# Kernel tuning notes

Measured on AMD Instinct MI355X. Metric: run time of the kernel, lower is better.

Reference implementation:

```python
import jax, jax.numpy as jnp
import numpy as np
from math import sqrt

HEAD_DIM = 128
MASKED = True


def setup_inputs() -> dict:
    key = jax.random.key(0)
    kq, kk, kv = jax.random.split(key, 3)
    B, S, D = 16, 2048, HEAD_DIM
    return {
        "queries": jax.random.normal(kq, (B, S, D), dtype=jnp.float32),
        "keys": jax.random.normal(kk, (B, S, D), dtype=jnp.float32),
        "values": jax.random.normal(kv, (B, S, D), dtype=jnp.float32),
    }


def reference(queries, keys, values):
    # scores: (B, Sq, Sk)
    scores = jnp.einsum("bqd,bkd->bqk", queries, keys) / sqrt(HEAD_DIM)
    if MASKED:
        # Faithful to torch.tril: upper-triangular entries set to 0.0
        # (NOT -inf) BEFORE softmax — reproduces the original's
        # multiplicative mask semantics exactly.
        scores = jnp.tril(scores)
    weights = jax.nn.softmax(scores, axis=-1)
    return jnp.einsum("bqk,bkd->bqd", weights, values)
```

## Files before the change

### kernel.cpp

```cpp
#include <hip/hip_runtime.h>
#include <hip/hip_bf16.h>

#define DEVI static __device__ __forceinline__

typedef __attribute__((ext_vector_type(8))) short short8;
typedef __attribute__((ext_vector_type(16))) float f32x16;
typedef __attribute__((ext_vector_type(2))) unsigned int uintx2;

#define S_LEN 2048
#define D_DIM 128
#define NBATCH 16
#define QSC ((float)(0.08838834764831845 * 1.4426950408889634))
#define MFIX 8.0f
#define E8 0.00390625f

#if __has_builtin(__builtin_amdgcn_exp2f)
#define EXP2(x) __builtin_amdgcn_exp2f(x)
#else
#define EXP2(x) exp2f(x)
#endif

DEVI unsigned short f2bf(float x) {
  union { float f; unsigned int u; } a; a.f = x;
  unsigned int u = a.u;
  unsigned int r = (u + 0x7fffu + ((u >> 16) & 1u)) >> 16;
  return (unsigned short)r;
}

DEVI unsigned int cvtpk(float lo, float hi) {
  unsigned int r;
  asm volatile("v_cvt_pk_bf16_f32 %0, %1, %2" : "=v"(r) : "v"(lo), "v"(hi));
  return r;
}

DEVI void plswap(unsigned int& a, unsigned int& b) {
  uintx2 r = __builtin_amdgcn_permlane32_swap(a, b, false, false);
  a = r[0];
  b = r[1];
}

DEVI float xhalf_sum(float x) {
  union { float f; unsigned int u; } a, b;
  a.f = x; b.f = x;
  plswap(a.u, b.u);
  return a.f + b.f;
}


__global__ void prep(const float* __restrict__ K, const float* __restrict__ V,
                     unsigned short* __restrict__ Kb, unsigned short* __restrict__ Vt,
                     float* __restrict__ Tsum) {
  __shared__ unsigned short t[64][68];
  const int tt = threadIdx.x;
  if (blockIdx.x >= 1024) {
    const int M4 = (NBATCH * S_LEN * D_DIM) / 4;
    for (int i = (blockIdx.x - 1024) * 256 + tt; i < M4; i += 2048 * 256) {
      const size_t idx = (size_t)i * 4;
      const float4 v = *reinterpret_cast<const float4*>(K + idx);
      ushort4 o;
      o.x = f2bf(v.x); o.y = f2bf(v.y); o.z = f2bf(v.z); o.w = f2bf(v.w);
      *reinterpret_cast<ushort4*>(Kb + idx) = o;
    }
    return;
  }
  const int bid = blockIdx.x;
  const int b = bid >> 6, rem = bid & 63;
  const int st = rem & 31, s0 = st * 64, d0 = (rem >> 5) * 64;
  const int r = tt >> 2, c = (tt & 3) * 16;
  const float* src = V + ((size_t)(b * S_LEN + s0 + r)) * D_DIM + d0 + c;
#pragma unroll
  for (int i = 0; i < 4; i++) {
    float4 v = reinterpret_cast<const float4*>(src)[i];
    t[r][c + 4 * i + 0] = f2bf(v.x);
    t[r][c + 4 * i + 1] = f2bf(v.y);
    t[r][c + 4 * i + 2] = f2bf(v.z);
    t[r][c + 4 * i + 3] = f2bf(v.w);
  }
  __syncthreads();
  unsigned short* dst = Vt + (((size_t)(b * 32 + st)) * 128 + d0 + r) * 64 + c;
#pragma unroll
  for (int i = 0; i < 4; i++) {
    ushort4 o;
    o.x = t[c + 4 * i + 0][r];
    o.y = t[c + 4 * i + 1][r];
    o.z = t[c + 4 * i + 2][r];
    o.w = t[c + 4 * i + 3][r];
    reinterpret_cast<ushort4*>(dst)[i] = o;
  }
  if (tt < 64) {
    float s = 0.0f;
#pragma unroll 8
    for (int rr = 0; rr < 64; rr++) {
      union { float f; unsigned int u; } cv;
      cv.u = ((unsigned int)t[rr][tt]) << 16;
      s += cv.f;
    }
    Tsum[((size_t)b * 32 + st) * 128 + d0 + tt] = s;
  }
}

__global__ void sufB(const float* __restrict__ Tsum, float* __restrict__ SufV) {
  const int b = blockIdx.x;
  const int d = threadIdx.x;
  float v[32];
#pragma unroll
  for (int t = 0; t < 32; t++) v[t] = Tsum[((size_t)b * 32 + t) * 128 + d];
  float run = 0.0f;
  SufV[((size_t)b * 33 + 32) * 128 + d] = 0.0f;
#pragma unroll
  for (int t = 31; t >= 0; t--) {
    run += v[t];
    SufV[((size_t)b * 33 + t) * 128 + d] = run;
  }
}


#define AS1 __attribute__((address_space(1)))
#define AS3 __attribute__((address_space(3)))

DEVI short8 ldK(const char* ldsK, int row, int off) {
  int addr = row * 256 + (off ^ ((row & 15) << 4));
  return *reinterpret_cast<const short8*>(ldsK + addr);
}
DEVI short8 ldV(const char* ldsV, int row, int off) {
  int addr = row * 128 + (off ^ ((row & 7) << 4));
  return *reinterpret_cast<const short8*>(ldsV + addr);
}

template <bool MASK>
DEVI void tile_body(const char* cb, const short8* qf, f32x16 (&acc)[4],
                    float& l_run, const int ln31, const int h, const int kh,
                    const int qrow, const int kvb) {
  f32x16 sT;
#pragma unroll
  for (int r = 0; r < 16; r++) sT[r] = 0.0f;
  __builtin_amdgcn_s_setprio(1);
#pragma unroll
  for (int kf = 0; kf < 8; kf++) {
    short8 af = ldK(cb, ln31 + 32 * kh, 32 * kf + 16 * h);
    sT = __builtin_amdgcn_mfma_f32_32x32x16_bf16(af, qf[kf], sT, 0, 0, 0);
  }
  __builtin_amdgcn_s_setprio(0);
  if (MASK) {
#pragma unroll
    for (int r = 0; r < 16; r++) {
      int kvg = kvb + (r & 3) + 8 * (r >> 2) + 4 * h;
      if (kvg > qrow) sT[r] = 0.0f;
    }
  }
#pragma unroll
  for (int r = 0; r < 16; r++) sT[r] = EXP2(sT[r] - MFIX);
  float ts[8];
#pragma unroll
  for (int r = 0; r < 8; r++) ts[r] = sT[r] + sT[r + 8];
#pragma unroll
  for (int r = 0; r < 4; r++) ts[r] = ts[r] + ts[r + 4];
  float sum = (ts[0] + ts[1]) + (ts[2] + ts[3]);
  sum = xhalf_sum(sum);
  l_run += sum;
#pragma unroll
  for (int kl = 0; kl < 2; kl++) {
    const int ra = 8 * kl;
    const int rb = 8 * kl + 4;
    unsigned int a0 = cvtpk(sT[ra + 0], sT[ra + 1]);
    unsigned int a1 = cvtpk(sT[ra + 2], sT[ra + 3]);
    unsigned int b0 = cvtpk(sT[rb + 0], sT[rb + 1]);
    unsigned int b1 = cvtpk(sT[rb + 2], sT[rb + 3]);
    plswap(a0, b0);
    plswap(a1, b1);
    union { short8 v; unsigned int u[4]; } pa;
    pa.u[0] = a0; pa.u[1] = a1; pa.u[2] = b0; pa.u[3] = b1;
    const int vboff = 64 * kh + 32 * kl + 16 * h;
    __builtin_amdgcn_s_setprio(1);
#pragma unroll
    for (int nt = 0; nt < 4; nt++) {
      short8 vb = ldV(cb + 16384, ln31 + 32 * nt, vboff);
      acc[nt] = __builtin_amdgcn_mfma_f32_32x32x16_bf16(pa.v, vb, acc[nt], 0, 0, 0);
    }
    __builtin_amdgcn_s_setprio(0);
  }
}

#define SMEM_BYTES 132096

struct WaveCtx {
  int w, lane, ln31, h, qs, grp, kh, tsel, dstpart;
  int off[8];
  const char* tbase;
};

DEVI void stage_tile(char* smem, const WaveCtx& c, int t, int j, int bi) {
  if (t <= j) {
    const char* src = c.tbase + (size_t)t * 16384;
    const int dbase = bi * 65536 + c.tsel * 32768 + c.dstpart;
#pragma unroll
    for (int i = 0; i < 8; i++) {
      __builtin_amdgcn_global_load_lds((const AS1 unsigned int*)(src + c.off[i]),
                                       (AS3 unsigned int*)(smem + dbase + i * 1024),
                                       16, 0, 0);
    }
  }
}

DEVI void run_strip(int j, int b, char* smem, const WaveCtx& c,
                    const float* __restrict__ Q, const float* __restrict__ SufV,
                    float* __restrict__ out) {
  const int q0 = j * 64;
  const int kv_end = q0 + 64;
  const int qrow = q0 + 32 * c.qs + c.ln31;

  short8 qf[8];
  {
    const float* qsrc = Q + ((size_t)b * S_LEN + qrow) * D_DIM + 8 * c.h;
#pragma unroll
    for (int kf = 0; kf < 8; kf++) {
      float4 a = *reinterpret_cast<const float4*>(qsrc + 16 * kf);
      float4 d = *reinterpret_cast<const float4*>(qsrc + 16 * kf + 4);
      union { short8 v; unsigned int u[4]; } q8;
      q8.u[0] = cvtpk(a.x * QSC, a.y * QSC);
      q8.u[1] = cvtpk(a.z * QSC, a.w * QSC);
      q8.u[2] = cvtpk(d.x * QSC, d.y * QSC);
      q8.u[3] = cvtpk(d.z * QSC, d.w * QSC);
      qf[kf] = q8.v;
    }
  }

  f32x16 acc[4];
#pragma unroll
  for (int nt = 0; nt < 4; nt++)
#pragma unroll
    for (int rr = 0; rr < 16; rr++) acc[nt][rr] = 0.0f;
  float l_run = 0.0f;

  const int nph = (j >> 1) + 1;
  stage_tile(smem, c, c.tsel, j, 0);
  __syncthreads();
  int bi = 0;
  for (int ph = 0; ph < nph; ph++) {
    if (ph + 1 < nph) stage_tile(smem, c, 2 * (ph + 1) + c.tsel, j, bi ^ 1);
    const int t = 2 * ph + c.grp;
    if (t <= j) {
      const char* cb = smem + bi * 65536 + c.grp * 32768;
      if (t == j)
        tile_body<true>(cb, qf, acc, l_run, c.ln31, c.h, c.kh, qrow,
                        t * 64 + 32 * c.kh);
      else
        tile_body<false>(cb, qf, acc, l_run, c.ln31, c.h, c.kh, qrow,
                         t * 64 + 32 * c.kh);
    }
    __syncthreads();
    bi ^= 1;
  }

  float* pbase = (float*)smem + c.w * 4096;
#pragma unroll
  for (int nt = 0; nt < 4; nt++)
#pragma unroll
    for (int rr = 0; rr < 16; rr++) {
      int cr = (rr & 3) + 8 * (rr >> 2) + 4 * c.h;
      pbase[cr * 128 + c.ln31 + 32 * nt] = acc[nt][rr];
    }
  float* lbase = (float*)(smem + 131072) + c.w * 32;
  if (c.h == 0) lbase[c.ln31] = l_run;
  __syncthreads();

  const int s = c.w & 3;
  const float* P0 = (float*)smem + (c.qs * 4) * 4096;
  const float* L0 = (float*)(smem + 131072) + (c.qs * 4) * 32;
  float l_tot = L0[c.ln31] + L0[32 + c.ln31] + L0[64 + c.ln31] + L0[96 + c.ln31];
  l_tot += (float)(S_LEN - kv_end) * E8;
  const float svv = SufV[((size_t)b * 33 + (kv_end >> 6)) * 128 + 32 * s + c.ln31];
  float* ob = out + ((size_t)b * S_LEN + q0 + 32 * c.qs) * D_DIM + 32 * s + c.ln31;
#pragma unroll
  for (int rr = 0; rr < 16; rr++) {
    int cr = (rr & 3) + 8 * (rr >> 2) + 4 * c.h;
    int cidx = cr * 128 + 32 * s + c.ln31;
    float v = P0[cidx] + P0[4096 + cidx] + P0[8192 + cidx] + P0[12288 + cidx];
    float lq = __shfl(l_tot, cr);
    ob[(size_t)cr * D_DIM] = (v + E8 * svv) / lq;
  }
  __syncthreads();
}

__global__ __launch_bounds__(512, 2) void attn_kernel(
    const float* __restrict__ Q, const unsigned short* __restrict__ Kb,
    const unsigned short* __restrict__ Vt, const float* __restrict__ SufV,
    float* __restrict__ out) {
  __shared__ __align__(16) char smem[SMEM_BYTES];

  WaveCtx c;
  const int tid = threadIdx.x;
  c.w = tid >> 6;
  c.lane = tid & 63;
  c.ln31 = c.lane & 31;
  c.h = c.lane >> 5;
  c.qs = c.w >> 2;
  c.grp = (c.w >> 1) & 1;
  c.kh = c.w & 1;
  c.tsel = c.w >> 2;
  const int part = c.w & 3;

  const int bid = blockIdx.x;
  const int x = bid & 7, idx = bid >> 3;
  const int b = 2 * x + (idx & 1);
  const int p = idx >> 1;

  if (part < 2) {
#pragma unroll
    for (int i = 0; i < 8; i++) {
      int L = (part * 8 + i) * 1024 + c.lane * 16;
      int row = L >> 8;
      c.off[i] = row * 256 + ((L & 255) ^ ((row & 15) << 4));
    }
    c.tbase = (const char*)(Kb + (size_t)b * S_LEN * D_DIM);
    c.dstpart = part * 8192;
  } else {
#pragma unroll
    for (int i = 0; i < 8; i++) {
      int L = ((part - 2) * 8 + i) * 1024 + c.lane * 16;
      int row = L >> 7;
      c.off[i] = (L & ~127) + ((L & 127) ^ ((row & 7) << 4));
    }
    c.tbase = (const char*)Vt + (size_t)b * (S_LEN * D_DIM * 2);
    c.dstpart = 16384 + (part - 2) * 8192;
  }

  run_strip(31 - p, b, smem, c, Q, SufV, out);
  run_strip(p, b, smem, c, Q, SufV, out);
}


extern "C" void kernel_launch(void* const* d_in, const int* in_sizes, int n_in,
                              void* d_out, int out_size, void* d_ws, size_t ws_size,
                              hipStream_t stream) {
  const float* Q = (const float*)d_in[0];
  const float* K = (const float*)d_in[1];
  const float* V = (const float*)d_in[2];
  float* out = (float*)d_out;

  char* ws = (char*)d_ws;
  unsigned short* Kb = (unsigned short*)ws;
  unsigned short* Vt = Kb + 4194304;
  float* Tsum = (float*)(ws + 16777216);
  float* SufV = Tsum + 65536;

  prep<<<3072, 256, 0, stream>>>(K, V, Kb, Vt, Tsum);
  sufB<<<16, 128, 0, stream>>>(Tsum, SufV);
  attn_kernel<<<256, 512, 0, stream>>>(Q, Kb, Vt, SufV, out);
}
```

Before: 53.12 us.

## Split paired causal strips into one-strip 256-thread blocks with single-tile pipeline

The old kernel ran 512-thread blocks that each processed two complementary query strips (31-p and p), with two wave groups working on alternate key tiles and a 4-way cross-wave reduction through LDS. The new kernel launches 512 blocks of 256 threads, one strip per block, streams one K/V tile at a time with double buffering, and reduces only two key-halves, adding one partial directly from registers. This halves LDS use and shrinks the epilogue reduction. The cost is that per-block work now varies a lot across causal strips, so load balance depends on the hardware scheduler, and each wave walks twice as many tiles serially.

```diff
diff --git a/kernel.cpp b/kernel.cpp
--- a/kernel.cpp
+++ b/kernel.cpp
@@ -181,37 +181,67 @@
   }
 }
 
-#define SMEM_BYTES 132096
-
-struct WaveCtx {
-  int w, lane, ln31, h, qs, grp, kh, tsel, dstpart;
+#define SMEM_BYTES 66048
+
+__global__ __launch_bounds__(256, 2) void attn_kernel(
+    const float* __restrict__ Q, const unsigned short* __restrict__ Kb,
+    const unsigned short* __restrict__ Vt, const float* __restrict__ SufV,
+    float* __restrict__ out) {
+  __shared__ __align__(16) char smem[SMEM_BYTES];
+
+  const int tid = threadIdx.x;
+  const int w = tid >> 6, lane = tid & 63;
+  const int ln31 = lane & 31, h = lane >> 5;
+  const int kh = w & 1;
+  const int qh = w >> 1;
+
+  const int bid = blockIdx.x;
+  const int x = bid & 7, idx = bid >> 3;
+  const int b = 2 * x + (idx & 1);
+  const int j = 31 - (idx >> 1);
+
+  const int q0 = j * 64;
+  const int kv_end = q0 + 64;
+  const int qrow = q0 + 32 * qh + ln31;
+
   int off[8];
   const char* tbase;
-};
-
-DEVI void stage_tile(char* smem, const WaveCtx& c, int t, int j, int bi) {
-  if (t <= j) {
-    const char* src = c.tbase + (size_t)t * 16384;
-    const int dbase = bi * 65536 + c.tsel * 32768 + c.dstpart;
+  int dstpart;
+  if (w < 2) {
 #pragma unroll
     for (int i = 0; i < 8; i++) {
-      __builtin_amdgcn_global_load_lds((const AS1 unsigned int*)(src + c.off[i]),
-                                       (AS3 unsigned int*)(smem + dbase + i * 1024),
-                                       16, 0, 0);
-    }
-  }
-}
-
-DEVI void run_strip(int j, int b, char* smem, const WaveCtx& c,
-                    const float* __restrict__ Q, const float* __restrict__ SufV,
-                    float* __restrict__ out) {
-  const int q0 = j * 64;
-  const int kv_end = q0 + 64;
-  const int qrow = q0 + 32 * c.qs + c.ln31;
+      int L = (w * 8 + i) * 1024 + lane * 16;
+      int row = L >> 8;
+      off[i] = row * 256 + ((L & 255) ^ ((row & 15) << 4));
+    }
+    tbase = (const char*)(Kb + (size_t)b * S_LEN * D_DIM);
+    dstpart = w * 8192;
+  } else {
+#pragma unroll
+    for (int i = 0; i < 8; i++) {
+      int L = ((w - 2) * 8 + i) * 1024 + lane * 16;
+      int row = L >> 7;
+      off[i] = (L & ~127) + ((L & 127) ^ ((row & 7) << 4));
+    }
+    tbase = (const char*)Vt + (size_t)b * (S_LEN * D_DIM * 2);
+    dstpart = 16384 + (w - 2) * 8192;
+  }
+
+#define STAGE(t, bufb)                                                         \
+  do {                                                                         \
+    const char* src_ = tbase + (size_t)(t) * 16384;                            \
+    const int d0_ = (bufb) + dstpart;                                          \
+    _Pragma("unroll")                                                          \
+    for (int i = 0; i < 8; i++) {                                              \
+      __builtin_amdgcn_global_load_lds((const AS1 unsigned int*)(src_ + off[i]),\
+                                       (AS3 unsigned int*)(smem + d0_ + i * 1024),\
+                                       16, 0, 0);                              \
+    }                                                                          \
+  } while (0)
 
   short8 qf[8];
   {
-    const float* qsrc = Q + ((size_t)b * S_LEN + qrow) * D_DIM + 8 * c.h;
+    const float* qsrc = Q + ((size_t)b * S_LEN + qrow) * D_DIM + 8 * h;
 #pragma unroll
     for (int kf = 0; kf < 8; kf++) {
       float4 a = *reinterpret_cast<const float4*>(qsrc + 16 * kf);
@@ -232,101 +262,53 @@
     for (int rr = 0; rr < 16; rr++) acc[nt][rr] = 0.0f;
   float l_run = 0.0f;
 
-  const int nph = (j >> 1) + 1;
-  stage_tile(smem, c, c.tsel, j, 0);
+  STAGE(0, 0);
   __syncthreads();
-  int bi = 0;
-  for (int ph = 0; ph < nph; ph++) {
-    if (ph + 1 < nph) stage_tile(smem, c, 2 * (ph + 1) + c.tsel, j, bi ^ 1);
-    const int t = 2 * ph + c.grp;
-    if (t <= j) {
-      const char* cb = smem + bi * 65536 + c.grp * 32768;
-      if (t == j)
-        tile_body<true>(cb, qf, acc, l_run, c.ln31, c.h, c.kh, qrow,
-                        t * 64 + 32 * c.kh);
-      else
-        tile_body<false>(cb, qf, acc, l_run, c.ln31, c.h, c.kh, qrow,
-                         t * 64 + 32 * c.kh);
+  int buf = 0;
+  for (int kt = 0; kt <= j; kt++) {
+    const int bb = buf << 15;
+    if (kt < j) {
+      STAGE(kt + 1, bb ^ 32768);
+      tile_body<false>(smem + bb, qf, acc, l_run, ln31, h, kh, qrow,
+                       kt * 64 + 32 * kh);
+    } else {
+      tile_body<true>(smem + bb, qf, acc, l_run, ln31, h, kh, qrow,
+                      kt * 64 + 32 * kh);
     }
     __syncthreads();
-    bi ^= 1;
-  }
-
-  float* pbase = (float*)smem + c.w * 4096;
-#pragma unroll
-  for (int nt = 0; nt < 4; nt++)
-#pragma unroll
-    for (int rr = 0; rr < 16; rr++) {
-      int cr = (rr & 3) + 8 * (rr >> 2) + 4 * c.h;
-      pbase[cr * 128 + c.ln31 + 32 * nt] = acc[nt][rr];
-    }
-  float* lbase = (float*)(smem + 131072) + c.w * 32;
-  if (c.h == 0) lbase[c.ln31] = l_run;
+    buf ^= 1;
+  }
+
+  float* pbase = (float*)smem + qh * 4096;
+  float* lbase = (float*)(smem + 32768) + qh * 32;
+  if (kh == 1) {
+#pragma unroll
+    for (int nt = 0; nt < 4; nt++)
+#pragma unroll
+      for (int rr = 0; rr < 16; rr++) {
+        int cr = (rr & 3) + 8 * (rr >> 2) + 4 * h;
+        pbase[cr * 128 + ln31 + 32 * nt] = acc[nt][rr];
+      }
+    if (h == 0) lbase[ln31] = l_run;
+  }
   __syncthreads();
-
-  const int s = c.w & 3;
-  const float* P0 = (float*)smem + (c.qs * 4) * 4096;
-  const float* L0 = (float*)(smem + 131072) + (c.qs * 4) * 32;
-  float l_tot = L0[c.ln31] + L0[32 + c.ln31] + L0[64 + c.ln31] + L0[96 + c.ln31];
-  l_tot += (float)(S_LEN - kv_end) * E8;
-  const float svv = SufV[((size_t)b * 33 + (kv_end >> 6)) * 128 + 32 * s + c.ln31];
-  float* ob = out + ((size_t)b * S_LEN + q0 + 32 * c.qs) * D_DIM + 32 * s + c.ln31;
-#pragma unroll
-  for (int rr = 0; rr < 16; rr++) {
-    int cr = (rr & 3) + 8 * (rr >> 2) + 4 * c.h;
-    int cidx = cr * 128 + 32 * s + c.ln31;
-    float v = P0[cidx] + P0[4096 + cidx] + P0[8192 + cidx] + P0[12288 + cidx];
-    float lq = __shfl(l_tot, cr);
-    ob[(size_t)cr * D_DIM] = (v + E8 * svv) / lq;
-  }
-  __syncthreads();
-}
-
-__global__ __launch_bounds__(512, 2) void attn_kernel(
-    const float* __restrict__ Q, const unsigned short* __restrict__ Kb,
-    const unsigned short* __restrict__ Vt, const float* __restrict__ SufV,
-    float* __restrict__ out) {
-  __shared__ __align__(16) char smem[SMEM_BYTES];
-
-  WaveCtx c;
-  const int tid = threadIdx.x;
-  c.w = tid >> 6;
-  c.lane = tid & 63;
-  c.ln31 = c.lane & 31;
-  c.h = c.lane >> 5;
-  c.qs = c.w >> 2;
-  c.grp = (c.w >> 1) & 1;
-  c.kh = c.w & 1;
-  c.tsel = c.w >> 2;
-  const int part = c.w & 3;
-
-  const int bid = blockIdx.x;
-  const int x = bid & 7, idx = bid >> 3;
-  const int b = 2 * x + (idx & 1);
-  const int p = idx >> 1;
-
-  if (part < 2) {
-#pragma unroll
-    for (int i = 0; i < 8; i++) {
-      int L = (part * 8 + i) * 1024 + c.lane * 16;
-      int row = L >> 8;
-      c.off[i] = row * 256 + ((L & 255) ^ ((row & 15) << 4));
-    }
-    c.tbase = (const char*)(Kb + (size_t)b * S_LEN * D_DIM);
-    c.dstpart = part * 8192;
-  } else {
-#pragma unroll
-    for (int i = 0; i < 8; i++) {
-      int L = ((part - 2) * 8 + i) * 1024 + c.lane * 16;
-      int row = L >> 7;
-      c.off[i] = (L & ~127) + ((L & 127) ^ ((row & 7) << 4));
-    }
-    c.tbase = (const char*)Vt + (size_t)b * (S_LEN * D_DIM * 2);
-    c.dstpart = 16384 + (part - 2) * 8192;
-  }
-
-  run_strip(31 - p, b, smem, c, Q, SufV, out);
-  run_strip(p, b, smem, c, Q, SufV, out);
+  if (kh == 0) {
+    float l_tot = l_run + lbase[ln31];
+    l_tot += (float)(S_LEN - kv_end) * E8;
+    const float* sv = SufV + ((size_t)b * 33 + (kv_end >> 6)) * 128;
+    float* ob = out + ((size_t)b * S_LEN + q0 + 32 * qh) * D_DIM + ln31;
+#pragma unroll
+    for (int nt = 0; nt < 4; nt++) {
+      float svv = sv[ln31 + 32 * nt];
+#pragma unroll
+      for (int rr = 0; rr < 16; rr++) {
+        int cr = (rr & 3) + 8 * (rr >> 2) + 4 * h;
+        float v = acc[nt][rr] + pbase[cr * 128 + ln31 + 32 * nt] + E8 * svv;
+        float lq = __shfl(l_tot, cr);
+        ob[(size_t)cr * D_DIM + 32 * nt] = v / lq;
+      }
+    }
+  }
 }
 
 
@@ -346,5 +328,5 @@
 
   prep<<<3072, 256, 0, stream>>>(K, V, Kb, Vt, Tsum);
   sufB<<<16, 128, 0, stream>>>(Tsum, SufV);
-  attn_kernel<<<256, 512, 0, stream>>>(Q, Kb, Vt, SufV, out);
-}
+  attn_kernel<<<512, 256, 0, stream>>>(Q, Kb, Vt, SufV, out);
+}
```

New measurement: 62.73 us. 18.1% more time.

## Overlap next-tile async loads with compute using partial vmcnt waits

Applied to the files above, without the earlier changes.

Makes every phase unconditionally issue the next K/V tile load into the alternate LDS buffer, clamping out-of-range tiles to the last valid one so the count of in-flight loads stays uniform. A partial s_waitcnt vmcnt(8) then waits only for the current tile's loads, and raw s_barrier replaces __syncthreads, so the prefetch can stay in flight across the compute. It also splits the QK^T MFMA chain into two independent accumulators to shorten the dependency chain. The clamped loads add redundant global traffic at the tail, and correctness depends on the hand-written waitcnt and barrier ordering being right.

```diff
diff --git a/kernel.cpp b/kernel.cpp
--- a/kernel.cpp
+++ b/kernel.cpp
@@ -131,16 +131,21 @@
 DEVI void tile_body(const char* cb, const short8* qf, f32x16 (&acc)[4],
                     float& l_run, const int ln31, const int h, const int kh,
                     const int qrow, const int kvb) {
+  f32x16 sA, sB;
+#pragma unroll
+  for (int r = 0; r < 16; r++) { sA[r] = 0.0f; sB[r] = 0.0f; }
+  __builtin_amdgcn_s_setprio(1);
+#pragma unroll
+  for (int kf = 0; kf < 8; kf += 2) {
+    short8 a0 = ldK(cb, ln31 + 32 * kh, 32 * kf + 16 * h);
+    short8 a1 = ldK(cb, ln31 + 32 * kh, 32 * (kf + 1) + 16 * h);
+    sA = __builtin_amdgcn_mfma_f32_32x32x16_bf16(a0, qf[kf], sA, 0, 0, 0);
+    sB = __builtin_amdgcn_mfma_f32_32x32x16_bf16(a1, qf[kf + 1], sB, 0, 0, 0);
+  }
+  __builtin_amdgcn_s_setprio(0);
   f32x16 sT;
 #pragma unroll
-  for (int r = 0; r < 16; r++) sT[r] = 0.0f;
-  __builtin_amdgcn_s_setprio(1);
-#pragma unroll
-  for (int kf = 0; kf < 8; kf++) {
-    short8 af = ldK(cb, ln31 + 32 * kh, 32 * kf + 16 * h);
-    sT = __builtin_amdgcn_mfma_f32_32x32x16_bf16(af, qf[kf], sT, 0, 0, 0);
-  }
-  __builtin_amdgcn_s_setprio(0);
+  for (int r = 0; r < 16; r++) sT[r] = sA[r] + sB[r];
   if (MASK) {
 #pragma unroll
     for (int r = 0; r < 16; r++) {
@@ -189,16 +194,14 @@
   const char* tbase;
 };
 
-DEVI void stage_tile(char* smem, const WaveCtx& c, int t, int j, int bi) {
-  if (t <= j) {
-    const char* src = c.tbase + (size_t)t * 16384;
-    const int dbase = bi * 65536 + c.tsel * 32768 + c.dstpart;
-#pragma unroll
-    for (int i = 0; i < 8; i++) {
-      __builtin_amdgcn_global_load_lds((const AS1 unsigned int*)(src + c.off[i]),
-                                       (AS3 unsigned int*)(smem + dbase + i * 1024),
-                                       16, 0, 0);
-    }
+DEVI void stage_tile(char* smem, const WaveCtx& c, int t, int bi) {
+  const char* src = c.tbase + (size_t)t * 16384;
+  const int dbase = bi * 65536 + c.tsel * 32768 + c.dstpart;
+#pragma unroll
+  for (int i = 0; i < 8; i++) {
+    __builtin_amdgcn_global_load_lds((const AS1 unsigned int*)(src + c.off[i]),
+                                     (AS3 unsigned int*)(smem + dbase + i * 1024),
+                                     16, 0, 0);
   }
 }
 
@@ -233,11 +236,20 @@
   float l_run = 0.0f;
 
   const int nph = (j >> 1) + 1;
-  stage_tile(smem, c, c.tsel, j, 0);
-  __syncthreads();
+  {
+    int t0 = c.tsel;
+    if (t0 > j) t0 = j;
+    stage_tile(smem, c, t0, 0);
+  }
   int bi = 0;
   for (int ph = 0; ph < nph; ph++) {
-    if (ph + 1 < nph) stage_tile(smem, c, 2 * (ph + 1) + c.tsel, j, bi ^ 1);
+    int tn = 2 * (ph + 1) + c.tsel;
+    if (tn > j) tn = j;
+    stage_tile(smem, c, tn, bi ^ 1);
+    asm volatile("s_waitcnt vmcnt(8)" ::: "memory");
+    __builtin_amdgcn_sched_barrier(0);
+    __builtin_amdgcn_s_barrier();
+    __builtin_amdgcn_sched_barrier(0);
     const int t = 2 * ph + c.grp;
     if (t <= j) {
       const char* cb = smem + bi * 65536 + c.grp * 32768;
@@ -248,9 +260,11 @@
         tile_body<false>(cb, qf, acc, l_run, c.ln31, c.h, c.kh, qrow,
                          t * 64 + 32 * c.kh);
     }
-    __syncthreads();
+    __builtin_amdgcn_s_barrier();
+    __builtin_amdgcn_sched_barrier(0);
     bi ^= 1;
   }
+  __syncthreads();
 
   float* pbase = (float*)smem + c.w * 4096;
 #pragma unroll
```

After: 55.62 us. +4.7%, slower.

## Stage 128-key K/V tiles per phase with four key-quarter waves per query half

Applied to the files above, without the earlier changes.

Reorganizes the Vt transpose layout into 128-key blocks and loads a full 128-row K tile plus matching V tile per pipeline phase, so each of four waves per query half processes a 32-key quarter. LDS address offsets for K and V fragments are precomputed per thread into arrays. This aims to halve the number of phases and barriers per strip and simplify the staging logic. The causal skip now works at 32-key granularity within larger tiles, and the precomputed offset arrays add register pressure. A stray extern declaration is left in.

```diff
diff --git a/kernel.cpp b/kernel.cpp
--- a/kernel.cpp
+++ b/kernel.cpp
@@ -77,7 +77,8 @@
     t[r][c + 4 * i + 3] = f2bf(v.w);
   }
   __syncthreads();
-  unsigned short* dst = Vt + (((size_t)(b * 32 + st)) * 128 + d0 + r) * 64 + c;
+  unsigned short* dst =
+      Vt + (((size_t)(b * 16 + (st >> 1))) * 128 + d0 + r) * 128 + (st & 1) * 64 + c;
 #pragma unroll
   for (int i = 0; i < 4; i++) {
     ushort4 o;
@@ -118,26 +119,17 @@
 #define AS1 __attribute__((address_space(1)))
 #define AS3 __attribute__((address_space(3)))
 
-DEVI short8 ldK(const char* ldsK, int row, int off) {
-  int addr = row * 256 + (off ^ ((row & 15) << 4));
-  return *reinterpret_cast<const short8*>(ldsK + addr);
-}
-DEVI short8 ldV(const char* ldsV, int row, int off) {
-  int addr = row * 128 + (off ^ ((row & 7) << 4));
-  return *reinterpret_cast<const short8*>(ldsV + addr);
-}
-
 template <bool MASK>
-DEVI void tile_body(const char* cb, const short8* qf, f32x16 (&acc)[4],
-                    float& l_run, const int ln31, const int h, const int kh,
-                    const int qrow, const int kvb) {
+DEVI void tile_body(const char* kb, const char* vb, const int* ka, const int* va,
+                    const short8* qf, f32x16 (&acc)[4], float& l_run,
+                    const int h, const int qrow, const int kvb) {
   f32x16 sT;
 #pragma unroll
   for (int r = 0; r < 16; r++) sT[r] = 0.0f;
   __builtin_amdgcn_s_setprio(1);
 #pragma unroll
   for (int kf = 0; kf < 8; kf++) {
-    short8 af = ldK(cb, ln31 + 32 * kh, 32 * kf + 16 * h);
+    short8 af = *reinterpret_cast<const short8*>(kb + ka[kf]);
     sT = __builtin_amdgcn_mfma_f32_32x32x16_bf16(af, qf[kf], sT, 0, 0, 0);
   }
   __builtin_amdgcn_s_setprio(0);
@@ -170,12 +162,11 @@
     plswap(a1, b1);
     union { short8 v; unsigned int u[4]; } pa;
     pa.u[0] = a0; pa.u[1] = a1; pa.u[2] = b0; pa.u[3] = b1;
-    const int vboff = 64 * kh + 32 * kl + 16 * h;
     __builtin_amdgcn_s_setprio(1);
 #pragma unroll
     for (int nt = 0; nt < 4; nt++) {
-      short8 vb = ldV(cb + 16384, ln31 + 32 * nt, vboff);
-      acc[nt] = __builtin_amdgcn_mfma_f32_32x32x16_bf16(pa.v, vb, acc[nt], 0, 0, 0);
+      short8 vf = *reinterpret_cast<const short8*>(vb + va[kl * 4 + nt]);
+      acc[nt] = __builtin_amdgcn_mfma_f32_32x32x16_bf16(pa.v, vf, acc[nt], 0, 0, 0);
     }
     __builtin_amdgcn_s_setprio(0);
   }
@@ -184,21 +175,19 @@
 #define SMEM_BYTES 132096
 
 struct WaveCtx {
-  int w, lane, ln31, h, qs, grp, kh, tsel, dstpart;
+  int w, lane, ln31, h, qs, kq, dstpart;
   int off[8];
+  int ka[8];
+  int va[8];
   const char* tbase;
 };
 
-DEVI void stage_tile(char* smem, const WaveCtx& c, int t, int j, int bi) {
-  if (t <= j) {
-    const char* src = c.tbase + (size_t)t * 16384;
-    const int dbase = bi * 65536 + c.tsel * 32768 + c.dstpart;
-#pragma unroll
-    for (int i = 0; i < 8; i++) {
-      __builtin_amdgcn_global_load_lds((const AS1 unsigned int*)(src + c.off[i]),
-                                       (AS3 unsigned int*)(smem + dbase + i * 1024),
-                                       16, 0, 0);
-    }
+DEVI void stage_tile(char* smem, const WaveCtx& c, const char* src, int bb) {
+#pragma unroll
+  for (int i = 0; i < 8; i++) {
+    __builtin_amdgcn_global_load_lds(
+        (const AS1 unsigned int*)(src + c.off[i]),
+        (AS3 unsigned int*)(smem + bb + c.dstpart + i * 1024), 16, 0, 0);
   }
 }
 
@@ -208,6 +197,7 @@
   const int q0 = j * 64;
   const int kv_end = q0 + 64;
   const int qrow = q0 + 32 * c.qs + c.ln31;
+  const int T = (j >> 1) + 1;
 
   short8 qf[8];
   {
@@ -232,24 +222,27 @@
     for (int rr = 0; rr < 16; rr++) acc[nt][rr] = 0.0f;
   float l_run = 0.0f;
 
-  const int nph = (j >> 1) + 1;
-  stage_tile(smem, c, c.tsel, j, 0);
+  const char* kt0 = c.tbase;
+  const char* vt0 = c.tbase + 0;
+  (void)vt0; (void)kt0;
+
+  extern const char* __hip_unused;
+  stage_tile(smem, c, c.tbase + 0, 0);
   __syncthreads();
-  int bi = 0;
-  for (int ph = 0; ph < nph; ph++) {
-    if (ph + 1 < nph) stage_tile(smem, c, 2 * (ph + 1) + c.tsel, j, bi ^ 1);
-    const int t = 2 * ph + c.grp;
-    if (t <= j) {
-      const char* cb = smem + bi * 65536 + c.grp * 32768;
-      if (t == j)
-        tile_body<true>(cb, qf, acc, l_run, c.ln31, c.h, c.kh, qrow,
-                        t * 64 + 32 * c.kh);
+  for (int t = 0; t < T; t++) {
+    const int bb = (t & 1) << 16;
+    if (t + 1 < T)
+      stage_tile(smem, c, c.tbase + (size_t)(t + 1) * 32768, bb ^ 65536);
+    const int kbq = 128 * t + 32 * c.kq;
+    if (kbq < kv_end) {
+      const char* kb = smem + bb;
+      const char* vb = smem + bb + 32768;
+      if (kbq + 31 > q0 + 32 * c.qs)
+        tile_body<true>(kb, vb, c.ka, c.va, qf, acc, l_run, c.h, qrow, kbq);
       else
-        tile_body<false>(cb, qf, acc, l_run, c.ln31, c.h, c.kh, qrow,
-                         t * 64 + 32 * c.kh);
+        tile_body<false>(kb, vb, c.ka, c.va, qf, acc, l_run, c.h, qrow, kbq);
     }
     __syncthreads();
-    bi ^= 1;
   }
 
   float* pbase = (float*)smem + c.w * 4096;
@@ -295,34 +288,41 @@
   c.ln31 = c.lane & 31;
   c.h = c.lane >> 5;
   c.qs = c.w >> 2;
-  c.grp = (c.w >> 1) & 1;
-  c.kh = c.w & 1;
-  c.tsel = c.w >> 2;
-  const int part = c.w & 3;
+  c.kq = c.w & 3;
 
   const int bid = blockIdx.x;
   const int x = bid & 7, idx = bid >> 3;
   const int b = 2 * x + (idx & 1);
   const int p = idx >> 1;
 
-  if (part < 2) {
-#pragma unroll
-    for (int i = 0; i < 8; i++) {
-      int L = (part * 8 + i) * 1024 + c.lane * 16;
-      int row = L >> 8;
-      c.off[i] = row * 256 + ((L & 255) ^ ((row & 15) << 4));
-    }
+  const int part = c.w & 3;
+#pragma unroll
+  for (int i = 0; i < 8; i++) {
+    int L = (part * 8 + i) * 1024 + c.lane * 16;
+    int row = L >> 8;
+    c.off[i] = row * 256 + ((L & 255) ^ ((row & 15) << 4));
+  }
+  if (c.w < 4) {
     c.tbase = (const char*)(Kb + (size_t)b * S_LEN * D_DIM);
     c.dstpart = part * 8192;
   } else {
-#pragma unroll
-    for (int i = 0; i < 8; i++) {
-      int L = ((part - 2) * 8 + i) * 1024 + c.lane * 16;
-      int row = L >> 7;
-      c.off[i] = (L & ~127) + ((L & 127) ^ ((row & 7) << 4));
-    }
     c.tbase = (const char*)Vt + (size_t)b * (S_LEN * D_DIM * 2);
-    c.dstpart = 16384 + (part - 2) * 8192;
+    c.dstpart = 32768 + part * 8192;
+  }
+
+  {
+    const int krow = 32 * c.kq + c.ln31;
+    const int ksw = (krow & 15) << 4;
+#pragma unroll
+    for (int kf = 0; kf < 8; kf++)
+      c.ka[kf] = krow * 256 + ((32 * kf + 16 * c.h) ^ ksw);
+    const int vsw = (c.ln31 & 15) << 4;
+#pragma unroll
+    for (int kl = 0; kl < 2; kl++)
+#pragma unroll
+      for (int nt = 0; nt < 4; nt++)
+        c.va[kl * 4 + nt] = (c.ln31 + 32 * nt) * 256 +
+                            ((64 * c.kq + 32 * kl + 16 * c.h) ^ vsw);
   }
 
   run_strip(31 - p, b, smem, c, Q, SufV, out);
```

New measurement: 53.40 us. About the same (+0.5%).
